# Kernel optimization log

Hardware: AMD Instinct MI355X
Metric: run time of the kernel (lower is better)

The kernel has to match this reference:

```python
import jax, jax.numpy as jnp
import numpy as np
from jax import lax


def setup_inputs() -> dict:
    key = jax.random.key(0)
    k1, k2 = jax.random.split(key)
    B, Cin, T, H, W_ = 4, 16, 31, 128, 128
    Chid = 16
    inputs = jax.random.normal(k1, (B, Cin, T, H, W_), dtype=jnp.float32)
    # Conv3d(Cin, 2*Chid, kernel=3, padding=1) weights, OIDHW layout
    W = jax.random.normal(k2, (2 * Chid, Cin, 3, 3, 3), dtype=jnp.float32) * 0.05
    b = jnp.zeros((2 * Chid,), dtype=jnp.float32)
    return {"inputs": inputs, "W": W, "b": b}


def _fo_pool(Z, F):
    # Z, F: [B, C, T, H, W]; recurrence h_t = f_t * h_{t-1} + (1 - f_t) * z_t, h_{-1} = 0
    Zt = jnp.moveaxis(Z, 2, 0)  # [T, B, C, H, W]
    Ft = jnp.moveaxis(F, 2, 0)

    def step(h, zf):
        z, f = zf
        h = f * h + (1.0 - f) * z
        return h, h

    h0 = jnp.zeros_like(Zt[0])
    _, hs = lax.scan(step, h0, (Zt, Ft))
    return jnp.moveaxis(hs, 0, 2)  # back to [B, C, T, H, W]


def reference(inputs, W, b):
    # gated conv: Conv3d with SAME padding (kernel 3, padding 1)
    gates = lax.conv_general_dilated(
        inputs, W, window_strides=(1, 1, 1), padding="SAME",
        dimension_numbers=("NCDHW", "OIDHW", "NCDHW"))
    gates = gates + b[None, :, None, None, None]
    Chid = W.shape[0] // 2
    Z = jnp.tanh(gates[:, :Chid])
    F = jax.nn.sigmoid(gates[:, Chid:])
    return _fo_pool(Z, F)
```

## Files before the change

### kernel.cpp

```cpp
#include <hip/hip_runtime.h>
#include <cstdint>
#include <cstddef>

#define CIN     16
#define CHID    16
#define T_DIM   31
#define HW_     16384
#define CH_STRIDE 507904
#define TILE_H  4
#define TILE_W  32
#define SH      6
#define SW      34
#define SPOS    (SH * SW)
#define PSTR    24
#define SLICE_SH (SPOS * PSTR)

typedef short bf16x8 __attribute__((ext_vector_type(8)));
typedef float f32x16 __attribute__((ext_vector_type(16)));

__device__ __forceinline__ unsigned bf16_bits(float x) {
  unsigned u = __builtin_bit_cast(unsigned, x);
  u += 0x7FFFu + ((u >> 16) & 1u);
  return u >> 16;
}

__device__ __forceinline__ unsigned cvt_pk_bf16(float lo, float hi) {
  unsigned r;
  asm("v_cvt_pk_bf16_f32 %0, %1, %2" : "=v"(r) : "v"(lo), "v"(hi));
  return r;
}

__global__ __launch_bounds__(256, 2)
void qrnn3d_v4(const float* __restrict__ in, const float* __restrict__ Wg,
               const float* __restrict__ bg, float* __restrict__ out) {
  __shared__ short xs[4][SLICE_SH];

  const int tid  = threadIdx.x;
  const int bid  = blockIdx.x;
  const int b    = bid >> 7;
  const int tile = bid & 127;
  const int h0   = (tile >> 2) * TILE_H;
  const int w0   = (tile & 3) * TILE_W;

  const int lane = tid & 63;
  const int wid  = tid >> 6;
  const int col  = lane & 31;
  const int half = lane >> 5;

  bf16x8 wfrag[27];
#pragma unroll
  for (int tau = 0; tau < 27; ++tau) {
    bf16x8 f;
#pragma unroll
    for (int j = 0; j < 8; ++j)
      f[j] = (short)bf16_bits(Wg[col * 432 + (half * 8 + j) * 27 + tau]);
    wfrag[tau] = f;
  }

  f32x16 accInit;
  int voff[8];
#pragma unroll
  for (int r = 0; r < 8; ++r) {
    int oc = (r & 3) + 8 * (r >> 2) + 4 * half;
    accInit[r]     = bg[oc];
    accInit[r + 8] = bg[oc + 16];
    voff[r] = (b * CHID + oc) * CH_STRIDE + (h0 + wid) * 128 + (w0 + col);
  }

  const float* gp[4];
  int  lso[4];
  bool stv[4], ldv[4];
#pragma unroll
  for (int i = 0; i < 4; ++i) {
    int p   = tid + i * 256;
    int q   = p & 15;
    int c4  = (p >> 4) & 3;
    int j   = p >> 6;
    int pos = j * 16 + q;
    stv[i]  = (pos < SPOS);
    int hh  = pos / SW;
    int ww  = pos - hh * SW;
    int gh  = h0 + hh - 1, gw = w0 + ww - 1;
    ldv[i]  = stv[i] && ((unsigned)gh < 128u) && ((unsigned)gw < 128u);
    int sp  = ldv[i] ? (gh * 128 + gw) : 0;
    gp[i]   = in + (size_t)(b * CIN + c4 * 4) * CH_STRIDE + sp;
    lso[i]  = pos * PSTR + c4 * 4;
  }

#define LOADV(tz, vv)                                                \
  do {                                                               \
    if ((tz) <= 30) {                                                \
      const int toff = (tz) * HW_;                                   \
      _Pragma("unroll")                                              \
      for (int i = 0; i < 4; ++i) {                                  \
        _Pragma("unroll")                                            \
        for (int k = 0; k < 4; ++k)                                  \
          vv[i][k] = ldv[i] ? gp[i][toff + k * CH_STRIDE] : 0.0f;    \
      }                                                              \
    } else {                                                         \
      _Pragma("unroll")                                              \
      for (int i = 0; i < 4; ++i) {                                  \
        _Pragma("unroll")                                            \
        for (int k = 0; k < 4; ++k) vv[i][k] = 0.0f;                 \
      }                                                              \
    }                                                                \
  } while (0)

#define STOREV(vv, slot)                                             \
  do {                                                               \
    short* dst = &xs[(slot)][0];                                     \
    _Pragma("unroll")                                                \
    for (int i = 0; i < 4; ++i) {                                    \
      if (stv[i]) {                                                  \
        uint2 u;                                                     \
        u.x = cvt_pk_bf16(vv[i][0], vv[i][1]);                       \
        u.y = cvt_pk_bf16(vv[i][2], vv[i][3]);                       \
        *reinterpret_cast<uint2*>(dst + lso[i]) = u;                 \
      }                                                              \
    }                                                                \
  } while (0)

  int lb[9];
#pragma unroll
  for (int kh = 0; kh < 3; ++kh)
#pragma unroll
    for (int kw = 0; kw < 3; ++kw)
      lb[kh * 3 + kw] = ((wid + kh) * SW + (col + kw)) * PSTR + half * 8;

  float hst[8];
#pragma unroll
  for (int r = 0; r < 8; ++r) hst[r] = 0.0f;

  const float C_TANH = 2.8853900817779268f;
  const float C_SIG  = 1.4426950408889634f;

  auto compute = [&](int t) {
    const short* base = &xs[0][0];
    const short* sA = base + ((t + 3) & 3) * SLICE_SH;
    const short* sB = base + ((t    ) & 3) * SLICE_SH;
    const short* sC = base + ((t + 1) & 3) * SLICE_SH;

    f32x16 acc0 = accInit;
    f32x16 acc1;
#pragma unroll
    for (int i = 0; i < 16; ++i) acc1[i] = 0.0f;

#pragma unroll
    for (int kd = 0; kd < 3; ++kd) {
      const short* sp = (kd == 0) ? sA : (kd == 1) ? sB : sC;
#pragma unroll
      for (int u = 0; u < 9; ++u) {
        const int tau = kd * 9 + u;
        bf16x8 xb = *reinterpret_cast<const bf16x8*>(sp + lb[u]);
        if (tau & 1)
          acc1 = __builtin_amdgcn_mfma_f32_32x32x16_bf16(wfrag[tau], xb, acc1, 0, 0, 0);
        else
          acc0 = __builtin_amdgcn_mfma_f32_32x32x16_bf16(wfrag[tau], xb, acc0, 0, 0, 0);
      }
    }

    float* outT = out + (size_t)t * HW_;
#pragma unroll
    for (int r = 0; r < 8; ++r) {
      float zg = acc0[r] + acc1[r];
      float fg = acc0[r + 8] + acc1[r + 8];
      float ez = exp2f(zg * C_TANH);
      float z  = __builtin_fmaf(-2.0f, __builtin_amdgcn_rcpf(ez + 1.0f), 1.0f);
      float ef = exp2f(-fg * C_SIG);
      float f  = __builtin_amdgcn_rcpf(1.0f + ef);
      float h  = __builtin_fmaf(f, hst[r] - z, z);
      hst[r]   = h;
      outT[voff[r]] = h;
    }
  };

  float vA[4][4], vB[4][4];
  LOADV(0, vA); STOREV(vA, 0);
  LOADV(1, vA); STOREV(vA, 1);
  LOADV(2, vA);
  for (int i = tid; i < SLICE_SH / 2; i += 256)
    reinterpret_cast<unsigned*>(&xs[3][0])[i] = 0u;
  __syncthreads();

#pragma unroll 1
  for (int t = 0; t < 30; t += 2) {
    LOADV(t + 3, vB);
    STOREV(vA, (t + 2) & 3);
    compute(t);
    __syncthreads();
    LOADV(t + 4, vA);
    STOREV(vB, (t + 3) & 3);
    compute(t + 1);
    __syncthreads();
  }
  compute(30);

#undef LOADV
#undef STOREV
}

extern "C" void kernel_launch(void* const* d_in, const int* in_sizes, int n_in,
                              void* d_out, int out_size, void* d_ws, size_t ws_size,
                              hipStream_t stream) {
  const float* in = (const float*)d_in[0];
  const float* Wg = (const float*)d_in[1];
  const float* bg = (const float*)d_in[2];
  float* out      = (float*)d_out;
  (void)in_sizes; (void)n_in; (void)out_size; (void)d_ws; (void)ws_size;
  qrnn3d_v4<<<dim3(512), dim3(256), 0, stream>>>(in, Wg, bg, out);
}
```

Before: 129.0 us.

## Deepen LDS ring to six slots, halve barriers, precompute byte offsets

The shared-memory ring grows from 4 to 6 bf16 slices, so one barrier now covers two time steps instead of one, and the barrier waits only on LDS counters. Global load addresses become precomputed byte offsets, and out-of-range halo values are zeroed with a bitmask instead of a per-element predicate. Block IDs are remapped to interleave batches across XCDs, and outputs use nontemporal stores. LDS use per block goes up, which could affect occupancy at two blocks per CU, and the static slot schedule makes the code more complex.

```diff
diff --git a/kernel.cpp b/kernel.cpp
--- a/kernel.cpp
+++ b/kernel.cpp
@@ -14,6 +14,8 @@
 #define SPOS    (SH * SW)
 #define PSTR    24
 #define SLICE_SH (SPOS * PSTR)
+#define SLICE_B  (SLICE_SH * 2)
+#define NSLOT   6
 
 typedef short bf16x8 __attribute__((ext_vector_type(8)));
 typedef float f32x16 __attribute__((ext_vector_type(16)));
@@ -23,7 +25,6 @@
   u += 0x7FFFu + ((u >> 16) & 1u);
   return u >> 16;
 }
-
 __device__ __forceinline__ unsigned cvt_pk_bf16(float lo, float hi) {
   unsigned r;
   asm("v_cvt_pk_bf16_f32 %0, %1, %2" : "=v"(r) : "v"(lo), "v"(hi));
@@ -31,14 +32,15 @@
 }
 
 __global__ __launch_bounds__(256, 2)
-void qrnn3d_v4(const float* __restrict__ in, const float* __restrict__ Wg,
+void qrnn3d_v5(const float* __restrict__ in, const float* __restrict__ Wg,
                const float* __restrict__ bg, float* __restrict__ out) {
-  __shared__ short xs[4][SLICE_SH];
-
-  const int tid  = threadIdx.x;
-  const int bid  = blockIdx.x;
-  const int b    = bid >> 7;
-  const int tile = bid & 127;
+  __shared__ __align__(16) short xs[NSLOT][SLICE_SH];
+
+  const int tid = threadIdx.x;
+  const int bid = blockIdx.x;
+  const int lin  = ((bid & 7) << 6) | (bid >> 3);
+  const int b    = lin >> 7;
+  const int tile = lin & 127;
   const int h0   = (tile >> 2) * TILE_H;
   const int w0   = (tile & 3) * TILE_W;
 
@@ -58,145 +60,163 @@
   }
 
   f32x16 accInit;
-  int voff[8];
+  unsigned voffB[8];
 #pragma unroll
   for (int r = 0; r < 8; ++r) {
     int oc = (r & 3) + 8 * (r >> 2) + 4 * half;
     accInit[r]     = bg[oc];
     accInit[r + 8] = bg[oc + 16];
-    voff[r] = (b * CHID + oc) * CH_STRIDE + (h0 + wid) * 128 + (w0 + col);
-  }
-
-  const float* gp[4];
-  int  lso[4];
-  bool stv[4], ldv[4];
+    voffB[r] = (unsigned)(((b * CHID + oc) * CH_STRIDE + (h0 + wid) * 128 + (w0 + col)) * 4);
+  }
+
+  unsigned bo[16];
+  unsigned lwb[4];
+  unsigned msk[4];
+  bool stv3 = false;
 #pragma unroll
   for (int i = 0; i < 4; ++i) {
     int p   = tid + i * 256;
-    int q   = p & 15;
-    int c4  = (p >> 4) & 3;
-    int j   = p >> 6;
+    int q   = p & 15, c4 = (p >> 4) & 3, j = p >> 6;
     int pos = j * 16 + q;
-    stv[i]  = (pos < SPOS);
-    int hh  = pos / SW;
-    int ww  = pos - hh * SW;
-    int gh  = h0 + hh - 1, gw = w0 + ww - 1;
-    ldv[i]  = stv[i] && ((unsigned)gh < 128u) && ((unsigned)gw < 128u);
-    int sp  = ldv[i] ? (gh * 128 + gw) : 0;
-    gp[i]   = in + (size_t)(b * CIN + c4 * 4) * CH_STRIDE + sp;
-    lso[i]  = pos * PSTR + c4 * 4;
-  }
-
-#define LOADV(tz, vv)                                                \
-  do {                                                               \
-    if ((tz) <= 30) {                                                \
-      const int toff = (tz) * HW_;                                   \
-      _Pragma("unroll")                                              \
-      for (int i = 0; i < 4; ++i) {                                  \
-        _Pragma("unroll")                                            \
-        for (int k = 0; k < 4; ++k)                                  \
-          vv[i][k] = ldv[i] ? gp[i][toff + k * CH_STRIDE] : 0.0f;    \
-      }                                                              \
-    } else {                                                         \
-      _Pragma("unroll")                                              \
-      for (int i = 0; i < 4; ++i) {                                  \
-        _Pragma("unroll")                                            \
-        for (int k = 0; k < 4; ++k) vv[i][k] = 0.0f;                 \
-      }                                                              \
-    }                                                                \
-  } while (0)
-
-#define STOREV(vv, slot)                                             \
-  do {                                                               \
-    short* dst = &xs[(slot)][0];                                     \
-    _Pragma("unroll")                                                \
-    for (int i = 0; i < 4; ++i) {                                    \
-      if (stv[i]) {                                                  \
-        uint2 u;                                                     \
-        u.x = cvt_pk_bf16(vv[i][0], vv[i][1]);                       \
-        u.y = cvt_pk_bf16(vv[i][2], vv[i][3]);                       \
-        *reinterpret_cast<uint2*>(dst + lso[i]) = u;                 \
-      }                                                              \
-    }                                                                \
-  } while (0)
-
-  int lb[9];
-#pragma unroll
-  for (int kh = 0; kh < 3; ++kh)
-#pragma unroll
-    for (int kw = 0; kw < 3; ++kw)
-      lb[kh * 3 + kw] = ((wid + kh) * SW + (col + kw)) * PSTR + half * 8;
-
-  float hst[8];
-#pragma unroll
-  for (int r = 0; r < 8; ++r) hst[r] = 0.0f;
+    bool stvi = (pos < SPOS);
+    int hh = pos / SW, ww = pos - hh * SW;
+    int gh = h0 + hh - 1, gw = w0 + ww - 1;
+    bool ldvi = stvi && ((unsigned)gh < 128u) && ((unsigned)gw < 128u);
+    int sp = ldvi ? (gh * 128 + gw) : 0;
+#pragma unroll
+    for (int k = 0; k < 4; ++k)
+      bo[i * 4 + k] = (unsigned)(((b * CIN + c4 * 4 + k) * CH_STRIDE + sp) * 4);
+    lwb[i] = (unsigned)(pos * (PSTR * 2) + c4 * 8);
+    msk[i] = ldvi ? 0xFFFFFFFFu : 0u;
+    if (i == 3) stv3 = stvi;
+  }
+
+#define LOADV(TZ, vv) do {                                                  \
+    if ((TZ) <= 30) {                                                       \
+      const char* bp_ = (const char*)in + (size_t)(TZ) * 65536;             \
+      _Pragma("unroll") for (int i_ = 0; i_ < 4; ++i_) {                    \
+        _Pragma("unroll") for (int k_ = 0; k_ < 4; ++k_)                    \
+          vv[i_][k_] = *(const float*)(bp_ + bo[i_ * 4 + k_]);              \
+      }                                                                     \
+    } else {                                                                \
+      _Pragma("unroll") for (int i_ = 0; i_ < 4; ++i_) {                    \
+        _Pragma("unroll") for (int k_ = 0; k_ < 4; ++k_) vv[i_][k_] = 0.0f; \
+      }                                                                     \
+    }                                                                       \
+  } while (0)
+
+#define STOREV(vv, SLOTB) do {                                              \
+    char* dp_ = (char*)&xs[0][0] + (SLOTB);                                 \
+    _Pragma("unroll") for (int i_ = 0; i_ < 3; ++i_) {                      \
+      uint2 u_;                                                             \
+      u_.x = cvt_pk_bf16(vv[i_][0], vv[i_][1]) & msk[i_];                   \
+      u_.y = cvt_pk_bf16(vv[i_][2], vv[i_][3]) & msk[i_];                   \
+      *(uint2*)(dp_ + lwb[i_]) = u_;                                        \
+    }                                                                       \
+    if (stv3) {                                                             \
+      uint2 u_;                                                             \
+      u_.x = cvt_pk_bf16(vv[3][0], vv[3][1]) & msk[3];                      \
+      u_.y = cvt_pk_bf16(vv[3][2], vv[3][3]) & msk[3];                      \
+      *(uint2*)(dp_ + lwb[3]) = u_;                                         \
+    }                                                                       \
+  } while (0)
+
+  const unsigned lbB = (unsigned)((wid * SW + col) * (PSTR * 2) + half * 16);
+
+#define RD(SLOTB, U) (*(const bf16x8*)((const char*)&xs[0][0] + lbB + (SLOTB) + (((U) / 3) * SW + ((U) % 3)) * (PSTR * 2)))
 
   const float C_TANH = 2.8853900817779268f;
   const float C_SIG  = 1.4426950408889634f;
 
-  auto compute = [&](int t) {
-    const short* base = &xs[0][0];
-    const short* sA = base + ((t + 3) & 3) * SLICE_SH;
-    const short* sB = base + ((t    ) & 3) * SLICE_SH;
-    const short* sC = base + ((t + 1) & 3) * SLICE_SH;
-
-    f32x16 acc0 = accInit;
-    f32x16 acc1;
-#pragma unroll
-    for (int i = 0; i < 16; ++i) acc1[i] = 0.0f;
-
-#pragma unroll
-    for (int kd = 0; kd < 3; ++kd) {
-      const short* sp = (kd == 0) ? sA : (kd == 1) ? sB : sC;
-#pragma unroll
-      for (int u = 0; u < 9; ++u) {
-        const int tau = kd * 9 + u;
-        bf16x8 xb = *reinterpret_cast<const bf16x8*>(sp + lb[u]);
-        if (tau & 1)
-          acc1 = __builtin_amdgcn_mfma_f32_32x32x16_bf16(wfrag[tau], xb, acc1, 0, 0, 0);
-        else
-          acc0 = __builtin_amdgcn_mfma_f32_32x32x16_bf16(wfrag[tau], xb, acc0, 0, 0, 0);
-      }
-    }
-
-    float* outT = out + (size_t)t * HW_;
-#pragma unroll
-    for (int r = 0; r < 8; ++r) {
-      float zg = acc0[r] + acc1[r];
-      float fg = acc0[r + 8] + acc1[r + 8];
-      float ez = exp2f(zg * C_TANH);
-      float z  = __builtin_fmaf(-2.0f, __builtin_amdgcn_rcpf(ez + 1.0f), 1.0f);
-      float ef = exp2f(-fg * C_SIG);
-      float f  = __builtin_amdgcn_rcpf(1.0f + ef);
-      float h  = __builtin_fmaf(f, hst[r] - z, z);
-      hst[r]   = h;
-      outT[voff[r]] = h;
-    }
-  };
+  float hst[8];
+#pragma unroll
+  for (int r = 0; r < 8; ++r) hst[r] = 0.0f;
+
+#define COMPUTE(T, AB, BB, CB) do {                                          \
+    f32x16 acc1;                                                             \
+    _Pragma("unroll") for (int q_ = 0; q_ < 16; ++q_) acc1[q_] = 0.0f;       \
+    bf16x8 x0_ = RD(AB, 0);                                                  \
+    f32x16 acc0 = __builtin_amdgcn_mfma_f32_32x32x16_bf16(wfrag[0], x0_, accInit, 0, 0, 0); \
+    _Pragma("unroll") for (int u_ = 1; u_ < 9; ++u_) {                       \
+      bf16x8 xx_ = RD(AB, u_);                                               \
+      if (u_ & 1) acc1 = __builtin_amdgcn_mfma_f32_32x32x16_bf16(wfrag[u_], xx_, acc1, 0, 0, 0); \
+      else        acc0 = __builtin_amdgcn_mfma_f32_32x32x16_bf16(wfrag[u_], xx_, acc0, 0, 0, 0); \
+    }                                                                        \
+    _Pragma("unroll") for (int u_ = 0; u_ < 9; ++u_) {                       \
+      bf16x8 xx_ = RD(BB, u_);                                               \
+      if ((9 + u_) & 1) acc1 = __builtin_amdgcn_mfma_f32_32x32x16_bf16(wfrag[9 + u_], xx_, acc1, 0, 0, 0); \
+      else              acc0 = __builtin_amdgcn_mfma_f32_32x32x16_bf16(wfrag[9 + u_], xx_, acc0, 0, 0, 0); \
+    }                                                                        \
+    _Pragma("unroll") for (int u_ = 0; u_ < 9; ++u_) {                       \
+      bf16x8 xx_ = RD(CB, u_);                                               \
+      if ((18 + u_) & 1) acc1 = __builtin_amdgcn_mfma_f32_32x32x16_bf16(wfrag[18 + u_], xx_, acc1, 0, 0, 0); \
+      else               acc0 = __builtin_amdgcn_mfma_f32_32x32x16_bf16(wfrag[18 + u_], xx_, acc0, 0, 0, 0); \
+    }                                                                        \
+    const char* outp_ = (const char*)out + (size_t)(T) * 65536;              \
+    _Pragma("unroll") for (int r_ = 0; r_ < 8; ++r_) {                       \
+      float zg_ = acc0[r_] + acc1[r_];                                       \
+      float fg_ = acc0[r_ + 8] + acc1[r_ + 8];                               \
+      float ez_ = exp2f(zg_ * C_TANH);                                       \
+      float z_  = __builtin_fmaf(-2.0f, __builtin_amdgcn_rcpf(ez_ + 1.0f), 1.0f); \
+      float ef_ = exp2f(-fg_ * C_SIG);                                       \
+      float f_  = __builtin_amdgcn_rcpf(1.0f + ef_);                         \
+      float h_  = __builtin_fmaf(f_, hst[r_] - z_, z_);                      \
+      hst[r_]   = h_;                                                        \
+      __builtin_nontemporal_store(h_, (float*)(outp_ + voffB[r_]));          \
+    }                                                                        \
+  } while (0)
+
+#define BARRIER() do {                                                      \
+    asm volatile("s_waitcnt lgkmcnt(0)" ::: "memory");                      \
+    __builtin_amdgcn_s_barrier();                                           \
+    __builtin_amdgcn_sched_barrier(0);                                      \
+  } while (0)
 
   float vA[4][4], vB[4][4];
-  LOADV(0, vA); STOREV(vA, 0);
-  LOADV(1, vA); STOREV(vA, 1);
+  LOADV(0, vA);
+  LOADV(1, vB);
+  STOREV(vA, 0 * SLICE_B);
   LOADV(2, vA);
-  for (int i = tid; i < SLICE_SH / 2; i += 256)
-    reinterpret_cast<unsigned*>(&xs[3][0])[i] = 0u;
-  __syncthreads();
+  STOREV(vB, 1 * SLICE_B);
+  STOREV(vA, 2 * SLICE_B);
+  {
+    unsigned* zp = (unsigned*)&xs[5][0];
+    for (int i = tid; i < SLICE_SH / 2; i += 256) zp[i] = 0u;
+  }
+  BARRIER();
+  LOADV(3, vA);
 
 #pragma unroll 1
-  for (int t = 0; t < 30; t += 2) {
-    LOADV(t + 3, vB);
-    STOREV(vA, (t + 2) & 3);
-    compute(t);
-    __syncthreads();
-    LOADV(t + 4, vA);
-    STOREV(vB, (t + 3) & 3);
-    compute(t + 1);
-    __syncthreads();
-  }
-  compute(30);
+  for (int tb = 0; tb < 30; tb += 6) {
+    LOADV(tb + 4, vB);
+    STOREV(vA, 3 * SLICE_B);
+    COMPUTE(tb + 0, 5 * SLICE_B, 0 * SLICE_B, 1 * SLICE_B);
+    LOADV(tb + 5, vA);
+    STOREV(vB, 4 * SLICE_B);
+    COMPUTE(tb + 1, 0 * SLICE_B, 1 * SLICE_B, 2 * SLICE_B);
+    BARRIER();
+    LOADV(tb + 6, vB);
+    STOREV(vA, 5 * SLICE_B);
+    COMPUTE(tb + 2, 1 * SLICE_B, 2 * SLICE_B, 3 * SLICE_B);
+    LOADV(tb + 7, vA);
+    STOREV(vB, 0 * SLICE_B);
+    COMPUTE(tb + 3, 2 * SLICE_B, 3 * SLICE_B, 4 * SLICE_B);
+    BARRIER();
+    LOADV(tb + 8, vB);
+    STOREV(vA, 1 * SLICE_B);
+    COMPUTE(tb + 4, 3 * SLICE_B, 4 * SLICE_B, 5 * SLICE_B);
+    LOADV(tb + 9, vA);
+    if (tb + 5 <= 28) STOREV(vB, 2 * SLICE_B);
+    COMPUTE(tb + 5, 4 * SLICE_B, 5 * SLICE_B, 0 * SLICE_B);
+    BARRIER();
+  }
+  COMPUTE(30, 5 * SLICE_B, 0 * SLICE_B, 1 * SLICE_B);
 
 #undef LOADV
 #undef STOREV
+#undef RD
+#undef COMPUTE
+#undef BARRIER
 }
 
 extern "C" void kernel_launch(void* const* d_in, const int* in_sizes, int n_in,
@@ -207,5 +227,5 @@
   const float* bg = (const float*)d_in[2];
   float* out      = (float*)d_out;
   (void)in_sizes; (void)n_in; (void)out_size; (void)d_ws; (void)ws_size;
-  qrnn3d_v4<<<dim3(512), dim3(256), 0, stream>>>(in, Wg, bg, out);
-}
+  qrnn3d_v5<<<dim3(512), dim3(256), 0, stream>>>(in, Wg, bg, out);
+}
```

After: 150.4 us. 1.17x slower.

## Use single-wave workgroups per output row, drop barriers, swizzle block order

Applied to the files above, without the earlier changes.

Each workgroup becomes a single 64-lane wave that owns one output row of 32 pixels. It stages a 3x34 halo per time slice in LDS instead of a 6x34 tile shared by four waves. With only one wave per group the __syncthreads barriers are removed, and out-of-bounds loads are replaced by clamped unconditional loads plus bitmask zeroing. The block index is swizzled. The intent is to remove barrier stalls and expose more independent waves, at the cost of re-fetching halo rows (about 3x input reads instead of 1.5x) and more per-lane load work.

```diff
diff --git a/kernel.cpp b/kernel.cpp
--- a/kernel.cpp
+++ b/kernel.cpp
@@ -7,13 +7,12 @@
 #define T_DIM   31
 #define HW_     16384
 #define CH_STRIDE 507904
-#define TILE_H  4
 #define TILE_W  32
-#define SH      6
 #define SW      34
-#define SPOS    (SH * SW)
+#define SPOS    102
 #define PSTR    24
 #define SLICE_SH (SPOS * PSTR)
+#define NSLOT   4
 
 typedef short bf16x8 __attribute__((ext_vector_type(8)));
 typedef float f32x16 __attribute__((ext_vector_type(16)));
@@ -23,27 +22,25 @@
   u += 0x7FFFu + ((u >> 16) & 1u);
   return u >> 16;
 }
-
 __device__ __forceinline__ unsigned cvt_pk_bf16(float lo, float hi) {
   unsigned r;
   asm("v_cvt_pk_bf16_f32 %0, %1, %2" : "=v"(r) : "v"(lo), "v"(hi));
   return r;
 }
 
-__global__ __launch_bounds__(256, 2)
-void qrnn3d_v4(const float* __restrict__ in, const float* __restrict__ Wg,
+__global__ __launch_bounds__(64, 2)
+void qrnn3d_v9(const float* __restrict__ in, const float* __restrict__ Wg,
                const float* __restrict__ bg, float* __restrict__ out) {
-  __shared__ short xs[4][SLICE_SH];
-
-  const int tid  = threadIdx.x;
-  const int bid  = blockIdx.x;
-  const int b    = bid >> 7;
-  const int tile = bid & 127;
-  const int h0   = (tile >> 2) * TILE_H;
-  const int w0   = (tile & 3) * TILE_W;
-
-  const int lane = tid & 63;
-  const int wid  = tid >> 6;
+  __shared__ __align__(16) short xs[NSLOT][SLICE_SH];
+
+  const int lane = threadIdx.x;
+  const int wg   = blockIdx.x;
+  const int lin  = ((wg & 7) << 8) | (wg >> 3);
+  const int b    = lin >> 9;
+  const int rr   = lin & 511;
+  const int h    = rr >> 2;
+  const int w0   = (rr & 3) * TILE_W;
+
   const int col  = lane & 31;
   const int half = lane >> 5;
 
@@ -64,99 +61,92 @@
     int oc = (r & 3) + 8 * (r >> 2) + 4 * half;
     accInit[r]     = bg[oc];
     accInit[r + 8] = bg[oc + 16];
-    voff[r] = (b * CHID + oc) * CH_STRIDE + (h0 + wid) * 128 + (w0 + col);
-  }
-
-  const float* gp[4];
-  int  lso[4];
-  bool stv[4], ldv[4];
-#pragma unroll
-  for (int i = 0; i < 4; ++i) {
-    int p   = tid + i * 256;
-    int q   = p & 15;
-    int c4  = (p >> 4) & 3;
-    int j   = p >> 6;
-    int pos = j * 16 + q;
+    voff[r] = (b * CHID + oc) * CH_STRIDE + h * 128 + (w0 + col);
+  }
+
+  const float* gbase = in + (size_t)b * CIN * CH_STRIDE;
+  unsigned osp[7];
+  int  lwb[7];
+  unsigned msk[7];
+  bool stv[7];
+#pragma unroll
+  for (int i = 0; i < 7; ++i) {
+    int g   = lane + i * 64;
+    int c4  = g & 3;
+    int pos = g >> 2;
     stv[i]  = (pos < SPOS);
-    int hh  = pos / SW;
-    int ww  = pos - hh * SW;
-    int gh  = h0 + hh - 1, gw = w0 + ww - 1;
-    ldv[i]  = stv[i] && ((unsigned)gh < 128u) && ((unsigned)gw < 128u);
-    int sp  = ldv[i] ? (gh * 128 + gw) : 0;
-    gp[i]   = in + (size_t)(b * CIN + c4 * 4) * CH_STRIDE + sp;
-    lso[i]  = pos * PSTR + c4 * 4;
-  }
-
-#define LOADV(tz, vv)                                                \
-  do {                                                               \
-    if ((tz) <= 30) {                                                \
-      const int toff = (tz) * HW_;                                   \
-      _Pragma("unroll")                                              \
-      for (int i = 0; i < 4; ++i) {                                  \
-        _Pragma("unroll")                                            \
-        for (int k = 0; k < 4; ++k)                                  \
-          vv[i][k] = ldv[i] ? gp[i][toff + k * CH_STRIDE] : 0.0f;    \
-      }                                                              \
-    } else {                                                         \
-      _Pragma("unroll")                                              \
-      for (int i = 0; i < 4; ++i) {                                  \
-        _Pragma("unroll")                                            \
-        for (int k = 0; k < 4; ++k) vv[i][k] = 0.0f;                 \
-      }                                                              \
-    }                                                                \
+    int row = pos / SW, cw = pos - row * SW;
+    int gh  = h + row - 1, gw = w0 + cw - 1;
+    bool ok = stv[i] && ((unsigned)gh < 128u) && ((unsigned)gw < 128u);
+    osp[i]  = (unsigned)(c4 * 4 * CH_STRIDE + (ok ? gh * 128 + gw : 0));
+    lwb[i]  = pos * PSTR + c4 * 4;
+    msk[i]  = ok ? 0xFFFFFFFFu : 0u;
+  }
+
+#define LOADV(TZ, vv) do {                                                  \
+    if ((TZ) <= 30) {                                                       \
+      const float* bt_ = gbase + (TZ) * HW_;                                \
+      _Pragma("unroll") for (int i_ = 0; i_ < 7; ++i_) {                    \
+        _Pragma("unroll") for (int k_ = 0; k_ < 4; ++k_)                    \
+          vv[i_][k_] = bt_[osp[i_] + k_ * CH_STRIDE];                       \
+      }                                                                     \
+    } else {                                                                \
+      _Pragma("unroll") for (int i_ = 0; i_ < 7; ++i_) {                    \
+        _Pragma("unroll") for (int k_ = 0; k_ < 4; ++k_) vv[i_][k_] = 0.0f; \
+      }                                                                     \
+    }                                                                       \
   } while (0)
 
-#define STOREV(vv, slot)                                             \
-  do {                                                               \
-    short* dst = &xs[(slot)][0];                                     \
-    _Pragma("unroll")                                                \
-    for (int i = 0; i < 4; ++i) {                                    \
-      if (stv[i]) {                                                  \
-        uint2 u;                                                     \
-        u.x = cvt_pk_bf16(vv[i][0], vv[i][1]);                       \
-        u.y = cvt_pk_bf16(vv[i][2], vv[i][3]);                       \
-        *reinterpret_cast<uint2*>(dst + lso[i]) = u;                 \
-      }                                                              \
-    }                                                                \
+#define STOREV(vv, SLOT) do {                                               \
+    short* dp_ = &xs[(SLOT)][0];                                            \
+    _Pragma("unroll") for (int i_ = 0; i_ < 7; ++i_) {                      \
+      if (stv[i_]) {                                                        \
+        uint2 u_;                                                           \
+        u_.x = cvt_pk_bf16(vv[i_][0], vv[i_][1]) & msk[i_];                 \
+        u_.y = cvt_pk_bf16(vv[i_][2], vv[i_][3]) & msk[i_];                 \
+        *reinterpret_cast<uint2*>(dp_ + lwb[i_]) = u_;                      \
+      }                                                                     \
+    }                                                                       \
   } while (0)
 
-  int lb[9];
-#pragma unroll
-  for (int kh = 0; kh < 3; ++kh)
-#pragma unroll
-    for (int kw = 0; kw < 3; ++kw)
-      lb[kh * 3 + kw] = ((wid + kh) * SW + (col + kw)) * PSTR + half * 8;
-
-  float hst[8];
-#pragma unroll
-  for (int r = 0; r < 8; ++r) hst[r] = 0.0f;
+  const int lrd = col * PSTR + half * 8;
+
+#define RD(SP, U) (*(const bf16x8*)((SP) + lrd + (((U) / 3) * SW + ((U) % 3)) * PSTR))
 
   const float C_TANH = 2.8853900817779268f;
   const float C_SIG  = 1.4426950408889634f;
 
+  float hst[8];
+#pragma unroll
+  for (int r = 0; r < 8; ++r) hst[r] = 0.0f;
+
   auto compute = [&](int t) {
-    const short* base = &xs[0][0];
-    const short* sA = base + ((t + 3) & 3) * SLICE_SH;
-    const short* sB = base + ((t    ) & 3) * SLICE_SH;
-    const short* sC = base + ((t + 1) & 3) * SLICE_SH;
-
-    f32x16 acc0 = accInit;
+    const short* sA = &xs[(t + 3) & 3][0];
+    const short* sB = &xs[(t    ) & 3][0];
+    const short* sC = &xs[(t + 1) & 3][0];
+
     f32x16 acc1;
 #pragma unroll
     for (int i = 0; i < 16; ++i) acc1[i] = 0.0f;
-
-#pragma unroll
-    for (int kd = 0; kd < 3; ++kd) {
-      const short* sp = (kd == 0) ? sA : (kd == 1) ? sB : sC;
-#pragma unroll
-      for (int u = 0; u < 9; ++u) {
-        const int tau = kd * 9 + u;
-        bf16x8 xb = *reinterpret_cast<const bf16x8*>(sp + lb[u]);
-        if (tau & 1)
-          acc1 = __builtin_amdgcn_mfma_f32_32x32x16_bf16(wfrag[tau], xb, acc1, 0, 0, 0);
-        else
-          acc0 = __builtin_amdgcn_mfma_f32_32x32x16_bf16(wfrag[tau], xb, acc0, 0, 0, 0);
-      }
+    bf16x8 x0 = RD(sA, 0);
+    f32x16 acc0 = __builtin_amdgcn_mfma_f32_32x32x16_bf16(wfrag[0], x0, accInit, 0, 0, 0);
+#pragma unroll
+    for (int u = 1; u < 9; ++u) {
+      bf16x8 xb = RD(sA, u);
+      if (u & 1) acc1 = __builtin_amdgcn_mfma_f32_32x32x16_bf16(wfrag[u], xb, acc1, 0, 0, 0);
+      else       acc0 = __builtin_amdgcn_mfma_f32_32x32x16_bf16(wfrag[u], xb, acc0, 0, 0, 0);
+    }
+#pragma unroll
+    for (int u = 0; u < 9; ++u) {
+      bf16x8 xb = RD(sB, u);
+      if ((9 + u) & 1) acc1 = __builtin_amdgcn_mfma_f32_32x32x16_bf16(wfrag[9 + u], xb, acc1, 0, 0, 0);
+      else             acc0 = __builtin_amdgcn_mfma_f32_32x32x16_bf16(wfrag[9 + u], xb, acc0, 0, 0, 0);
+    }
+#pragma unroll
+    for (int u = 0; u < 9; ++u) {
+      bf16x8 xb = RD(sC, u);
+      if ((18 + u) & 1) acc1 = __builtin_amdgcn_mfma_f32_32x32x16_bf16(wfrag[18 + u], xb, acc1, 0, 0, 0);
+      else              acc0 = __builtin_amdgcn_mfma_f32_32x32x16_bf16(wfrag[18 + u], xb, acc0, 0, 0, 0);
     }
 
     float* outT = out + (size_t)t * HW_;
@@ -168,35 +158,35 @@
       float z  = __builtin_fmaf(-2.0f, __builtin_amdgcn_rcpf(ez + 1.0f), 1.0f);
       float ef = exp2f(-fg * C_SIG);
       float f  = __builtin_amdgcn_rcpf(1.0f + ef);
-      float h  = __builtin_fmaf(f, hst[r] - z, z);
-      hst[r]   = h;
-      outT[voff[r]] = h;
+      float hh = __builtin_fmaf(f, hst[r] - z, z);
+      hst[r]   = hh;
+      outT[voff[r]] = hh;
     }
   };
 
-  float vA[4][4], vB[4][4];
+  float vA[7][4], vB[7][4];
   LOADV(0, vA); STOREV(vA, 0);
   LOADV(1, vA); STOREV(vA, 1);
   LOADV(2, vA);
-  for (int i = tid; i < SLICE_SH / 2; i += 256)
-    reinterpret_cast<unsigned*>(&xs[3][0])[i] = 0u;
-  __syncthreads();
+  {
+    unsigned* zp = (unsigned*)&xs[3][0];
+    for (int i = lane; i < SLICE_SH / 2; i += 64) zp[i] = 0u;
+  }
 
 #pragma unroll 1
   for (int t = 0; t < 30; t += 2) {
     LOADV(t + 3, vB);
     STOREV(vA, (t + 2) & 3);
     compute(t);
-    __syncthreads();
     LOADV(t + 4, vA);
     STOREV(vB, (t + 3) & 3);
     compute(t + 1);
-    __syncthreads();
   }
   compute(30);
 
 #undef LOADV
 #undef STOREV
+#undef RD
 }
 
 extern "C" void kernel_launch(void* const* d_in, const int* in_sizes, int n_in,
@@ -207,5 +197,5 @@
   const float* bg = (const float*)d_in[2];
   float* out      = (float*)d_out;
   (void)in_sizes; (void)n_in; (void)out_size; (void)d_ws; (void)ws_size;
-  qrnn3d_v4<<<dim3(512), dim3(256), 0, stream>>>(in, Wg, bg, out);
-}
+  qrnn3d_v9<<<dim3(2048), dim3(64), 0, stream>>>(in, Wg, bg, out);
+}
```

New measurement: 506.5 us. +292.5%, slower.
